# Kernel tuning notes

Hardware: AMD Instinct MI355X
Metric: run time of the kernel (lower is better)

Reference implementation:

```python
import jax, jax.numpy as jnp
import numpy as np

B, H, W, DM = 32, 32, 32, 128   # batch, height, width, d_model
DIN, N, R = 64, 16, 8           # d_inner(low_dim), d_state, dt_rank=ceil(128/16)
LN_EPS = 1e-5


def setup_inputs() -> dict:
    key = jax.random.key(0)
    ks = jax.random.split(key, 10)
    x = jax.random.normal(ks[0], (B, H, W, DM), dtype=jnp.float32)
    w_in = jax.random.normal(ks[1], (2 * DIN, DM), dtype=jnp.float32) * 0.02
    conv_w = jax.random.normal(ks[2], (DIN, 1, 3, 3), dtype=jnp.float32) * 0.1
    conv_b = jax.random.normal(ks[3], (DIN,), dtype=jnp.float32) * 0.01
    xproj_w = jax.random.normal(ks[4], (R + 2 * N, DIN), dtype=jnp.float32) * 0.05
    dtproj_w = jax.random.uniform(ks[5], (DIN, R), dtype=jnp.float32,
                                  minval=-(R ** -0.5), maxval=R ** -0.5)
    # dt bias init: inverse-softplus of dt ~ LogUniform(1e-3, 0.1)
    dt = jnp.exp(jax.random.uniform(ks[6], (DIN,)) * (np.log(0.1) - np.log(0.001)) + np.log(0.001))
    dt = jnp.clip(dt, 1e-4, None)
    dtproj_b = dt + jnp.log(-jnp.expm1(-dt))
    A_logs = jnp.log(jnp.broadcast_to(jnp.arange(1, N + 1, dtype=jnp.float32), (DIN, N)))
    Ds = jnp.ones((DIN,), dtype=jnp.float32)
    ln_g = jnp.ones((DIN,), dtype=jnp.float32)
    ln_b = jnp.zeros((DIN,), dtype=jnp.float32)
    w_out = jax.random.normal(ks[7], (DM, DIN), dtype=jnp.float32) * 0.02
    return {"x": x, "w_in": w_in, "conv_w": conv_w, "conv_b": conv_b,
            "xproj_w": xproj_w, "dtproj_w": dtproj_w, "dtproj_b": dtproj_b,
            "A_logs": A_logs, "Ds": Ds, "ln_g": ln_g, "ln_b": ln_b, "w_out": w_out}


def _silu(v):
    return v * jax.nn.sigmoid(v)


def reference(x, w_in, conv_w, conv_b, xproj_w, dtproj_w, dtproj_b,
              A_logs, Ds, ln_g, ln_b, w_out):
    b, h, w, _ = x.shape
    L = h * w
    # in_proj (no bias) and gate split
    xz = jnp.einsum('bhwc,ec->bhwe', x, w_in)           # [B,H,W,2*DIN]
    xc, z = jnp.split(xz, 2, axis=-1)
    # depthwise conv2d, SAME padding (k=3, pad=1), then SiLU
    xc = jnp.transpose(xc, (0, 3, 1, 2))                # [B,DIN,H,W]
    xc = jax.lax.conv_general_dilated(
        xc, conv_w, window_strides=(1, 1), padding=((1, 1), (1, 1)),
        feature_group_count=DIN, dimension_numbers=('NCHW', 'OIHW', 'NCHW'))
    xc = _silu(xc + conv_b[None, :, None, None])
    u = xc.reshape(b, DIN, L)                            # [B,D,L]
    # x_proj -> dt, B, C
    x_dbl = jnp.einsum('bdl,cd->bcl', u, xproj_w)        # [B,R+2N,L]
    dts, Bs, Cs = x_dbl[:, :R], x_dbl[:, R:R + N], x_dbl[:, R + N:]
    delta = jnp.einsum('brl,dr->bdl', dts, dtproj_w) + dtproj_b[None, :, None]
    delta = jax.nn.softplus(delta)                       # [B,D,L]
    A = -jnp.exp(A_logs)                                 # [D,N]
    dA = jnp.exp(delta[..., None] * A[None, :, None, :])               # [B,D,L,N]
    dBu = (delta * u)[..., None] * jnp.swapaxes(Bs, 1, 2)[:, None]     # [B,D,L,N]
    # sequential selective scan over L
    dA_s = jnp.moveaxis(dA, 2, 0)                        # [L,B,D,N]
    dBu_s = jnp.moveaxis(dBu, 2, 0)
    C_s = jnp.moveaxis(Cs, 2, 0)                         # [L,B,N]

    def step(hst, inp):
        dA_t, dBu_t, C_t = inp
        hst = dA_t * hst + dBu_t                         # [B,D,N]
        y_t = jnp.einsum('bdn,bn->bd', hst, C_t)
        return hst, y_t

    h0 = jnp.zeros((b, DIN, N), dtype=u.dtype)
    _, ys = jax.lax.scan(step, h0, (dA_s, dBu_s, C_s))   # ys: [L,B,D]
    y = jnp.moveaxis(ys, 0, 2) + Ds[None, :, None] * u   # [B,D,L]
    # back to [B,H,W,D], layernorm, gate, out_proj
    y = jnp.swapaxes(y, 1, 2).reshape(b, h, w, DIN)
    mu = jnp.mean(y, axis=-1, keepdims=True)
    var = jnp.var(y, axis=-1, keepdims=True)
    y = (y - mu) * jax.lax.rsqrt(var + LN_EPS) * ln_g + ln_b
    y = y * _silu(z)
    return jnp.einsum('bhwd,cd->bhwc', y, w_out)
```

## Files before the change

kernel.cpp:

```cpp
#include <hip/hip_runtime.h>


typedef __attribute__((ext_vector_type(8))) short short8;
typedef __attribute__((ext_vector_type(4))) float floatx4;

__device__ __forceinline__ void cvt_split8(const float* v, short8& hi, short8& lo) {
#pragma unroll
    for (int i = 0; i < 8; ++i) {
        const unsigned xb = __float_as_uint(v[i]);
        hi[i] = (short)(xb >> 16);
        const float lf = v[i] - __uint_as_float(xb & 0xFFFF0000u);
        lo[i] = (short)(__float_as_uint(lf) >> 16);
    }
}

__global__ __launch_bounds__(256) void k1_gemm_in(
    const float* __restrict__ x, const float* __restrict__ w_in,
    float* __restrict__ xc, float* __restrict__ z)
{
    __shared__ float Cls[64 * 132];
    const int t    = threadIdx.x;
    const int p0   = blockIdx.x * 64;
    const int w    = t >> 6;
    const int l    = t & 63;
    const int lrow = l & 15, lk = l >> 4;
    const int m0   = w * 16;

    floatx4 acc[8];
#pragma unroll
    for (int nt = 0; nt < 8; ++nt) acc[nt] = (floatx4){0.f, 0.f, 0.f, 0.f};

#pragma unroll
    for (int ks = 0; ks < 4; ++ks) {
        const int k0 = ks * 32 + lk * 8;
        float av[8];
        {
            const float* ap = x + (size_t)(p0 + m0 + lrow) * 128 + k0;
            *reinterpret_cast<float4*>(&av[0]) = *reinterpret_cast<const float4*>(ap);
            *reinterpret_cast<float4*>(&av[4]) = *reinterpret_cast<const float4*>(ap + 4);
        }
        short8 ahi, alo;
        cvt_split8(av, ahi, alo);
#pragma unroll
        for (int nt = 0; nt < 8; ++nt) {
            float bv[8];
            const float* bp = w_in + (size_t)(nt * 16 + lrow) * 128 + k0;
            *reinterpret_cast<float4*>(&bv[0]) = *reinterpret_cast<const float4*>(bp);
            *reinterpret_cast<float4*>(&bv[4]) = *reinterpret_cast<const float4*>(bp + 4);
            short8 bhi, blo;
            cvt_split8(bv, bhi, blo);
            acc[nt] = __builtin_amdgcn_mfma_f32_16x16x32_bf16(ahi, bhi, acc[nt], 0, 0, 0);
            acc[nt] = __builtin_amdgcn_mfma_f32_16x16x32_bf16(ahi, blo, acc[nt], 0, 0, 0);
            acc[nt] = __builtin_amdgcn_mfma_f32_16x16x32_bf16(alo, bhi, acc[nt], 0, 0, 0);
        }
    }

#pragma unroll
    for (int nt = 0; nt < 8; ++nt)
#pragma unroll
        for (int r = 0; r < 4; ++r)
            Cls[(m0 + lk * 4 + r) * 132 + nt * 16 + lrow] = acc[nt][r];
    __syncthreads();

    const int b = p0 >> 10, lbase = p0 & 1023;
    {
        const int e  = t >> 2;
        const int pg = (t & 3) * 16;
        float tmp[16];
#pragma unroll
        for (int j = 0; j < 16; ++j) tmp[j] = Cls[(pg + j) * 132 + e];
        float* dst = xc + ((size_t)b * 64 + e) * 1024 + lbase + pg;
#pragma unroll
        for (int q = 0; q < 4; ++q)
            *reinterpret_cast<float4*>(dst + q * 4) =
                make_float4(tmp[q*4], tmp[q*4+1], tmp[q*4+2], tmp[q*4+3]);
    }
    {
        const int pix = t >> 2;
        const int dq  = (t & 3) * 16;
        const float* srcr = &Cls[pix * 132 + 64 + dq];
        float* dst = z + ((size_t)p0 + pix) * 64 + dq;
#pragma unroll
        for (int q = 0; q < 4; ++q)
            *reinterpret_cast<float4*>(dst + q * 4) =
                *reinterpret_cast<const float4*>(srcr + q * 4);
    }
}

__global__ __launch_bounds__(256) void k2_conv(
    const float* __restrict__ xc, const float* __restrict__ cw,
    const float* __restrict__ cb, float* __restrict__ u)
{
    __shared__ float pl[1024];
    const int bd = blockIdx.x;
    const int t  = threadIdx.x;
    const int d  = bd & 63;
    reinterpret_cast<float4*>(pl)[t] =
        reinterpret_cast<const float4*>(xc + (size_t)bd * 1024)[t];
    float w[9];
#pragma unroll
    for (int i = 0; i < 9; ++i) w[i] = cw[d * 9 + i];
    const float bias = cb[d];
    __syncthreads();
    float o[4];
#pragma unroll
    for (int i = 0; i < 4; ++i) {
        const int p  = t * 4 + i;
        const int py = p >> 5, px = p & 31;
        float s = 0.f;
#pragma unroll
        for (int ky = 0; ky < 3; ++ky) {
            const int iy = py + ky - 1;
            if (iy < 0 || iy > 31) continue;
#pragma unroll
            for (int kx = 0; kx < 3; ++kx) {
                const int ix = px + kx - 1;
                if (ix < 0 || ix > 31) continue;
                s = fmaf(pl[iy * 32 + ix], w[ky * 3 + kx], s);
            }
        }
        s += bias;
        o[i] = s / (1.f + __expf(-s));
    }
    reinterpret_cast<float4*>(u + (size_t)bd * 1024)[t] = make_float4(o[0], o[1], o[2], o[3]);
}

__global__ __launch_bounds__(64) void k3_xproj(
    const float* __restrict__ u, const float* __restrict__ xpw,
    const float* __restrict__ dtw_g, const float* __restrict__ dtb,
    float* __restrict__ delta, float* __restrict__ Bsp, float* __restrict__ Csp)
{
    __shared__ float ut[64][36];
    __shared__ float xw[64 * 40];
    __shared__ float xd8[8][36];
    __shared__ float dwv[64 * 9];
    const int t   = threadIdx.x;
    const int blk = blockIdx.x;
    const int b   = blk >> 5;
    const int l0  = (blk & 31) * 32;

#pragma unroll 4
    for (int c = 0; c < 40; ++c)
        xw[t * 40 + c] = xpw[(size_t)c * 64 + t];
#pragma unroll
    for (int k = 0; k < 8; ++k)
        dwv[t * 9 + k] = dtw_g[t * 8 + k];
    {
        const float* ub = u + (size_t)b * 65536 + l0;
#pragma unroll
        for (int i = t; i < 512; i += 64) {
            const int dd = i >> 3, pq = i & 7;
            const float4 v = *reinterpret_cast<const float4*>(ub + (size_t)dd * 1024 + pq * 4);
            *reinterpret_cast<float4*>(&ut[dd][pq * 4]) = v;
        }
    }
    __syncthreads();

    const int pixq = t & 7;
    const int cg   = t >> 3;
    const int c0   = cg * 5;
    float4 acc[5];
#pragma unroll
    for (int j = 0; j < 5; ++j) acc[j] = make_float4(0.f, 0.f, 0.f, 0.f);
#pragma unroll 8
    for (int dd = 0; dd < 64; ++dd) {
        const float4 uv = *reinterpret_cast<const float4*>(&ut[dd][pixq * 4]);
        const float* row = &xw[dd * 40 + c0];
#pragma unroll
        for (int j = 0; j < 5; ++j) {
            const float w = row[j];
            acc[j].x = fmaf(w, uv.x, acc[j].x);
            acc[j].y = fmaf(w, uv.y, acc[j].y);
            acc[j].z = fmaf(w, uv.z, acc[j].z);
            acc[j].w = fmaf(w, uv.w, acc[j].w);
        }
    }
#pragma unroll
    for (int j = 0; j < 5; ++j) {
        const int c = c0 + j;
        if (c < 8) {
            *reinterpret_cast<float4*>(&xd8[c][pixq * 4]) = acc[j];
        } else if (c < 24) {
            *reinterpret_cast<float4*>(Bsp + (size_t)b * 16384 +
                (size_t)(c - 8) * 1024 + l0 + pixq * 4) = acc[j];
        } else {
            *reinterpret_cast<float4*>(Csp + (size_t)b * 16384 +
                (size_t)(c - 24) * 1024 + l0 + pixq * 4) = acc[j];
        }
    }
    __syncthreads();

    const int dg = t >> 3;
    float dts[4][8];
#pragma unroll
    for (int e = 0; e < 4; ++e)
#pragma unroll
        for (int r = 0; r < 8; ++r)
            dts[e][r] = xd8[r][pixq * 4 + e];
    float* dp = delta + (size_t)b * 65536 + l0 + pixq * 4;
#pragma unroll
    for (int k = 0; k < 8; ++k) {
        const int dd = dg * 8 + k;
        const float* r8 = &dwv[dd * 9];
        const float bias = dtb[dd];
        float ov[4];
#pragma unroll
        for (int e = 0; e < 4; ++e) {
            float s = bias;
#pragma unroll
            for (int r = 0; r < 8; ++r) s = fmaf(dts[e][r], r8[r], s);
            ov[e] = fmaxf(s, 0.f) + log1pf(__expf(-fabsf(s)));
        }
        *reinterpret_cast<float4*>(dp + (size_t)dd * 1024) =
            make_float4(ov[0], ov[1], ov[2], ov[3]);
    }
}

__global__ __launch_bounds__(256) void k4_scan(
    const float* __restrict__ delta, const float* __restrict__ u,
    const float* __restrict__ Bsp, const float* __restrict__ Csp,
    const float* __restrict__ A_logs, const float* __restrict__ Ds,
    float* __restrict__ y)
{
    __shared__ float Ps[256][17];
    __shared__ float qs[256][17];
    __shared__ float Sp[16][17];
    __shared__ float Sq[16][17];
    const int t = threadIdx.x;
    const int pair = blockIdx.x;
    const int b = pair >> 6, d = pair & 63;

    float A[16];
#pragma unroll
    for (int n = 0; n < 16; ++n) A[n] = -__expf(A_logs[d * 16 + n]);

    const float4 d4 = *reinterpret_cast<const float4*>(delta + (size_t)pair * 1024 + t * 4);
    const float4 u4 = *reinterpret_cast<const float4*>(u     + (size_t)pair * 1024 + t * 4);
    const float du0 = d4.x * u4.x, du1 = d4.y * u4.y;
    const float du2 = d4.z * u4.z, du3 = d4.w * u4.w;

    const float* Bb = Bsp + (size_t)b * 16384 + t * 4;
    const float* Cb = Csp + (size_t)b * 16384 + t * 4;

#pragma unroll
    for (int n = 0; n < 16; ++n) {
        const float4 B4 = *reinterpret_cast<const float4*>(Bb + n * 1024);
        float a, P, q;
        a = __expf(d4.x * A[n]); P = a;   q = du0 * B4.x;
        a = __expf(d4.y * A[n]); P *= a;  q = fmaf(a, q, du1 * B4.y);
        a = __expf(d4.z * A[n]); P *= a;  q = fmaf(a, q, du2 * B4.z);
        a = __expf(d4.w * A[n]); P *= a;  q = fmaf(a, q, du3 * B4.w);
        Ps[t][n] = P; qs[t][n] = q;
    }
    __syncthreads();

    const int n = t >> 4, g = t & 15;
    float rp[16], rq[16];
    {
        float Pseg = 1.f, qseg = 0.f;
#pragma unroll
        for (int i = 0; i < 16; ++i) {
            const int c = g * 16 + i;
            rp[i] = Ps[c][n]; rq[i] = qs[c][n];
            qseg = fmaf(rp[i], qseg, rq[i]);
            Pseg *= rp[i];
        }
        Sp[g][n] = Pseg; Sq[g][n] = qseg;
    }
    __syncthreads();
    if (t < 16) {
        float h = 0.f;
#pragma unroll
        for (int s = 0; s < 16; ++s) {
            const float Pv = Sp[s][t], qv = Sq[s][t];
            Sp[s][t] = h;
            h = fmaf(Pv, h, qv);
        }
    }
    __syncthreads();
    {
        float h = Sp[g][n];
#pragma unroll
        for (int i = 0; i < 16; ++i) {
            const int c = g * 16 + i;
            qs[c][n] = h;
            h = fmaf(rp[i], h, rq[i]);
        }
    }
    __syncthreads();

    const float Dval = Ds[d];
    float y0 = Dval * u4.x, y1 = Dval * u4.y, y2 = Dval * u4.z, y3 = Dval * u4.w;
#pragma unroll
    for (int nn = 0; nn < 16; ++nn) {
        const float4 B4 = *reinterpret_cast<const float4*>(Bb + nn * 1024);
        const float4 C4 = *reinterpret_cast<const float4*>(Cb + nn * 1024);
        float h = qs[t][nn];
        float a;
        a = __expf(d4.x * A[nn]); h = fmaf(a, h, du0 * B4.x); y0 = fmaf(h, C4.x, y0);
        a = __expf(d4.y * A[nn]); h = fmaf(a, h, du1 * B4.y); y1 = fmaf(h, C4.y, y1);
        a = __expf(d4.z * A[nn]); h = fmaf(a, h, du2 * B4.z); y2 = fmaf(h, C4.z, y2);
        a = __expf(d4.w * A[nn]); h = fmaf(a, h, du3 * B4.w); y3 = fmaf(h, C4.w, y3);
    }
    *reinterpret_cast<float4*>(y + (size_t)pair * 1024 + t * 4) =
        make_float4(y0, y1, y2, y3);
}

__global__ __launch_bounds__(256) void k5_out(
    const float* __restrict__ y, const float* __restrict__ z,
    const float* __restrict__ ln_g, const float* __restrict__ ln_b,
    const float* __restrict__ w_out, float* __restrict__ out)
{
    __shared__ float yn[64 * 68];
    __shared__ float wo[64 * 132];
    const int t  = threadIdx.x;
    const int p0 = blockIdx.x * 64;
    const int b  = p0 >> 10, l0 = p0 & 1023;

    for (int i = t; i < 8192; i += 256) {
        const int c = i >> 6, dd = i & 63;
        wo[dd * 132 + c] = w_out[i];
    }

    {
        const int d = t >> 2;
        const float* yrow = y + ((size_t)b * 64 + d) * 1024 + l0;
#pragma unroll
        for (int k = 0; k < 4; ++k) {
            const int c4 = ((t & 3) + k * 4) * 4;
            const float4 v = *reinterpret_cast<const float4*>(&yrow[c4]);
            yn[(c4 + 0) * 68 + d] = v.x;
            yn[(c4 + 1) * 68 + d] = v.y;
            yn[(c4 + 2) * 68 + d] = v.z;
            yn[(c4 + 3) * 68 + d] = v.w;
        }
    }
    __syncthreads();

    const int lane = t & 63, wv = t >> 6;
    const float g = ln_g[lane], bbv = ln_b[lane];
#pragma unroll 1
    for (int i = 0; i < 16; ++i) {
        const int pl = wv * 16 + i;
        const size_t p = (size_t)p0 + pl;
        const float v  = yn[pl * 68 + lane];
        const float zv = z[p * 64 + lane];
        float s1 = v, s2 = v * v;
#pragma unroll
        for (int m = 1; m < 64; m <<= 1) {
            s1 += __shfl_xor(s1, m);
            s2 += __shfl_xor(s2, m);
        }
        const float mu   = s1 * (1.f / 64.f);
        const float var  = s2 * (1.f / 64.f) - mu * mu;
        const float rstd = rsqrtf(var + 1e-5f);
        const float sz   = zv / (1.f + __expf(-zv));
        yn[pl * 68 + lane] = ((v - mu) * rstd * g + bbv) * sz;
    }
    __syncthreads();

    const int tx = t & 31, ty = t >> 5;
    float acc[8][4];
#pragma unroll
    for (int i = 0; i < 8; ++i)
#pragma unroll
        for (int j = 0; j < 4; ++j) acc[i][j] = 0.f;

    for (int dd = 0; dd < 64; ++dd) {
        const float4 w4 = *reinterpret_cast<const float4*>(&wo[dd * 132 + (tx << 2)]);
#pragma unroll
        for (int i = 0; i < 8; ++i) {
            const float a = yn[(ty * 8 + i) * 68 + dd];
            acc[i][0] = fmaf(a, w4.x, acc[i][0]);
            acc[i][1] = fmaf(a, w4.y, acc[i][1]);
            acc[i][2] = fmaf(a, w4.z, acc[i][2]);
            acc[i][3] = fmaf(a, w4.w, acc[i][3]);
        }
    }
#pragma unroll
    for (int i = 0; i < 8; ++i) {
        const size_t p = (size_t)p0 + ty * 8 + i;
        *reinterpret_cast<float4*>(&out[p * 128 + (tx << 2)]) =
            make_float4(acc[i][0], acc[i][1], acc[i][2], acc[i][3]);
    }
}

extern "C" void kernel_launch(void* const* d_in, const int* in_sizes, int n_in,
                              void* d_out, int out_size, void* d_ws, size_t ws_size,
                              hipStream_t stream)
{
    const float* x        = (const float*)d_in[0];
    const float* w_in     = (const float*)d_in[1];
    const float* conv_w   = (const float*)d_in[2];
    const float* conv_b   = (const float*)d_in[3];
    const float* xproj_w  = (const float*)d_in[4];
    const float* dtproj_w = (const float*)d_in[5];
    const float* dtproj_b = (const float*)d_in[6];
    const float* A_logs   = (const float*)d_in[7];
    const float* Ds       = (const float*)d_in[8];
    const float* ln_g     = (const float*)d_in[9];
    const float* ln_b     = (const float*)d_in[10];
    const float* w_out    = (const float*)d_in[11];
    float* out = (float*)d_out;
    float* ws  = (float*)d_ws;

    const size_t M  = (size_t)2097152;
    float* xc    = ws;
    float* z     = ws + M;
    float* u     = ws + 2 * M;
    float* delta = ws + 3 * M;
    float* y     = ws + 4 * M;
    float* Bsp   = ws + 5 * M;
    float* Csp   = Bsp + 524288;

    k1_gemm_in<<<512, 256, 0, stream>>>(x, w_in, xc, z);
    k2_conv<<<2048, 256, 0, stream>>>(xc, conv_w, conv_b, u);
    k3_xproj<<<1024, 64, 0, stream>>>(u, xproj_w, dtproj_w, dtproj_b, delta, Bsp, Csp);
    k4_scan<<<2048, 256, 0, stream>>>(delta, u, Bsp, Csp, A_logs, Ds, y);
    k5_out<<<512, 256, 0, stream>>>(y, z, ln_g, ln_b, w_out, out);
}
```

Measured before the change: 103.7 us.

## Use split-bf16 MFMA for out_proj and cache scan decay factors

The out_proj GEMM in k5 moves from scalar FMA over an LDS-staged weight tile to MFMA 16x16x32 bf16 instructions. Both operands are split into hi/lo bf16 parts and three products are summed to keep near-fp32 accuracy, and the result is staged through LDS for coalesced stores. Weights are read directly from global memory instead of being transposed into shared memory. Separately, k4_scan keeps its 64 exp(delta*A) values in registers so the second pass reuses them instead of recomputing the exponentials, which adds register pressure.

```diff
diff --git a/kernel.cpp b/kernel.cpp
--- a/kernel.cpp
+++ b/kernel.cpp
@@ -230,10 +230,6 @@
     const int pair = blockIdx.x;
     const int b = pair >> 6, d = pair & 63;
 
-    float A[16];
-#pragma unroll
-    for (int n = 0; n < 16; ++n) A[n] = -__expf(A_logs[d * 16 + n]);
-
     const float4 d4 = *reinterpret_cast<const float4*>(delta + (size_t)pair * 1024 + t * 4);
     const float4 u4 = *reinterpret_cast<const float4*>(u     + (size_t)pair * 1024 + t * 4);
     const float du0 = d4.x * u4.x, du1 = d4.y * u4.y;
@@ -242,15 +238,22 @@
     const float* Bb = Bsp + (size_t)b * 16384 + t * 4;
     const float* Cb = Csp + (size_t)b * 16384 + t * 4;
 
+    float av[64];
 #pragma unroll
     for (int n = 0; n < 16; ++n) {
+        const float Aval = -__expf(A_logs[d * 16 + n]);
         const float4 B4 = *reinterpret_cast<const float4*>(Bb + n * 1024);
-        float a, P, q;
-        a = __expf(d4.x * A[n]); P = a;   q = du0 * B4.x;
-        a = __expf(d4.y * A[n]); P *= a;  q = fmaf(a, q, du1 * B4.y);
-        a = __expf(d4.z * A[n]); P *= a;  q = fmaf(a, q, du2 * B4.z);
-        a = __expf(d4.w * A[n]); P *= a;  q = fmaf(a, q, du3 * B4.w);
-        Ps[t][n] = P; qs[t][n] = q;
+        const float a0 = __expf(d4.x * Aval);
+        const float a1 = __expf(d4.y * Aval);
+        const float a2 = __expf(d4.z * Aval);
+        const float a3 = __expf(d4.w * Aval);
+        av[4*n+0] = a0; av[4*n+1] = a1; av[4*n+2] = a2; av[4*n+3] = a3;
+        float q = du0 * B4.x;
+        q = fmaf(a1, q, du1 * B4.y);
+        q = fmaf(a2, q, du2 * B4.z);
+        q = fmaf(a3, q, du3 * B4.w);
+        Ps[t][n] = a0 * a1 * a2 * a3;
+        qs[t][n] = q;
     }
     __syncthreads();
 
@@ -296,11 +299,10 @@
         const float4 B4 = *reinterpret_cast<const float4*>(Bb + nn * 1024);
         const float4 C4 = *reinterpret_cast<const float4*>(Cb + nn * 1024);
         float h = qs[t][nn];
-        float a;
-        a = __expf(d4.x * A[nn]); h = fmaf(a, h, du0 * B4.x); y0 = fmaf(h, C4.x, y0);
-        a = __expf(d4.y * A[nn]); h = fmaf(a, h, du1 * B4.y); y1 = fmaf(h, C4.y, y1);
-        a = __expf(d4.z * A[nn]); h = fmaf(a, h, du2 * B4.z); y2 = fmaf(h, C4.z, y2);
-        a = __expf(d4.w * A[nn]); h = fmaf(a, h, du3 * B4.w); y3 = fmaf(h, C4.w, y3);
+        h = fmaf(av[4*nn+0], h, du0 * B4.x); y0 = fmaf(h, C4.x, y0);
+        h = fmaf(av[4*nn+1], h, du1 * B4.y); y1 = fmaf(h, C4.y, y1);
+        h = fmaf(av[4*nn+2], h, du2 * B4.z); y2 = fmaf(h, C4.z, y2);
+        h = fmaf(av[4*nn+3], h, du3 * B4.w); y3 = fmaf(h, C4.w, y3);
     }
     *reinterpret_cast<float4*>(y + (size_t)pair * 1024 + t * 4) =
         make_float4(y0, y1, y2, y3);
@@ -312,15 +314,10 @@
     const float* __restrict__ w_out, float* __restrict__ out)
 {
     __shared__ float yn[64 * 68];
-    __shared__ float wo[64 * 132];
+    __shared__ float Cls[64 * 132];
     const int t  = threadIdx.x;
     const int p0 = blockIdx.x * 64;
     const int b  = p0 >> 10, l0 = p0 & 1023;
-
-    for (int i = t; i < 8192; i += 256) {
-        const int c = i >> 6, dd = i & 63;
-        wo[dd * 132 + c] = w_out[i];
-    }
 
     {
         const int d = t >> 2;
@@ -359,29 +356,53 @@
     }
     __syncthreads();
 
-    const int tx = t & 31, ty = t >> 5;
-    float acc[8][4];
-#pragma unroll
-    for (int i = 0; i < 8; ++i)
-#pragma unroll
-        for (int j = 0; j < 4; ++j) acc[i][j] = 0.f;
-
-    for (int dd = 0; dd < 64; ++dd) {
-        const float4 w4 = *reinterpret_cast<const float4*>(&wo[dd * 132 + (tx << 2)]);
-#pragma unroll
-        for (int i = 0; i < 8; ++i) {
-            const float a = yn[(ty * 8 + i) * 68 + dd];
-            acc[i][0] = fmaf(a, w4.x, acc[i][0]);
-            acc[i][1] = fmaf(a, w4.y, acc[i][1]);
-            acc[i][2] = fmaf(a, w4.z, acc[i][2]);
-            acc[i][3] = fmaf(a, w4.w, acc[i][3]);
-        }
-    }
-#pragma unroll
-    for (int i = 0; i < 8; ++i) {
-        const size_t p = (size_t)p0 + ty * 8 + i;
-        *reinterpret_cast<float4*>(&out[p * 128 + (tx << 2)]) =
-            make_float4(acc[i][0], acc[i][1], acc[i][2], acc[i][3]);
+    const int lrow = lane & 15, lk = lane >> 4;
+    const int m0   = wv * 16;
+    floatx4 acc[8];
+#pragma unroll
+    for (int nt = 0; nt < 8; ++nt) acc[nt] = (floatx4){0.f, 0.f, 0.f, 0.f};
+
+#pragma unroll
+    for (int ks = 0; ks < 2; ++ks) {
+        const int k0 = ks * 32 + lk * 8;
+        float av[8];
+        {
+            const float* ap = &yn[(m0 + lrow) * 68 + k0];
+            *reinterpret_cast<float4*>(&av[0]) = *reinterpret_cast<const float4*>(ap);
+            *reinterpret_cast<float4*>(&av[4]) = *reinterpret_cast<const float4*>(ap + 4);
+        }
+        short8 ahi, alo;
+        cvt_split8(av, ahi, alo);
+#pragma unroll
+        for (int nt = 0; nt < 8; ++nt) {
+            float bv[8];
+            const float* bp = w_out + (size_t)(nt * 16 + lrow) * 64 + k0;
+            *reinterpret_cast<float4*>(&bv[0]) = *reinterpret_cast<const float4*>(bp);
+            *reinterpret_cast<float4*>(&bv[4]) = *reinterpret_cast<const float4*>(bp + 4);
+            short8 bhi, blo;
+            cvt_split8(bv, bhi, blo);
+            acc[nt] = __builtin_amdgcn_mfma_f32_16x16x32_bf16(ahi, bhi, acc[nt], 0, 0, 0);
+            acc[nt] = __builtin_amdgcn_mfma_f32_16x16x32_bf16(ahi, blo, acc[nt], 0, 0, 0);
+            acc[nt] = __builtin_amdgcn_mfma_f32_16x16x32_bf16(alo, bhi, acc[nt], 0, 0, 0);
+        }
+    }
+
+#pragma unroll
+    for (int nt = 0; nt < 8; ++nt)
+#pragma unroll
+        for (int r = 0; r < 4; ++r)
+            Cls[(m0 + lk * 4 + r) * 132 + nt * 16 + lrow] = acc[nt][r];
+    __syncthreads();
+
+    {
+        const int pix = t >> 2;
+        const int dq  = (t & 3) * 32;
+        const float* srcr = &Cls[pix * 132 + dq];
+        float* dst = out + ((size_t)p0 + pix) * 128 + dq;
+#pragma unroll
+        for (int q = 0; q < 8; ++q)
+            *reinterpret_cast<float4*>(dst + q * 4) =
+                *reinterpret_cast<const float4*>(srcr + q * 4);
     }
 }
 
```

Result: slower. 107.8 us (+3.9%).
